# Kernel optimization log

Measured on AMD Instinct MI355X. Metric: run time of the kernel, lower is better.

## Reference

```python
import jax, jax.numpy as jnp
import numpy as np

B, L, D, H = 4, 1024, 768, 6
DH = D // H
EPS = 1e-5


def setup_inputs() -> dict:
    key = jax.random.key(0)
    kq, kk, kv, kl, kw = jax.random.split(key, 5)
    Q = jax.random.normal(kq, (B, L, D), jnp.float32)
    K = jax.random.normal(kk, (B, L, D), jnp.float32)
    V = jax.random.normal(kv, (B, L, D), jnp.float32)
    # realistic padding: each batch element has a valid length in [L//2, L]
    lengths = jax.random.randint(kl, (B,), L // 2, L + 1)
    valid = jnp.arange(L)[None, :] < lengths[:, None]          # (B, L)
    pad_mask = valid[:, :, None] & valid[:, None, :]           # (B, L, L), True = keep
    bx_packed = ~valid                                         # (B, L), True = padded
    # BatchNorm affine params (per-head channels)
    g1 = jnp.ones((H,), jnp.float32)
    b1 = jnp.zeros((H,), jnp.float32)
    g2 = jnp.ones((H,), jnp.float32)
    b2 = jnp.zeros((H,), jnp.float32)
    # posterior gate: Linear(H, 2)
    Wp = jax.random.normal(kw, (2, H), jnp.float32) * (1.0 / np.sqrt(H))
    bp = jnp.zeros((2,), jnp.float32)
    return {"Q": Q, "K": K, "V": V, "pad_mask": pad_mask, "bx_packed": bx_packed,
            "g1": g1, "b1": b1, "g2": g2, "b2": b2, "Wp": Wp, "bp": bp}


def _split_heads(x):
    b, l, _ = x.shape
    return x.reshape(b, l, H, DH).transpose(0, 2, 1, 3)  # (B, H, L, DH)


def _batchnorm(x, g, b):
    # x: (B, H, N); training-mode BatchNorm1d over channels H (stats over B and N)
    m = x.mean(axis=(0, 2), keepdims=True)
    v = x.var(axis=(0, 2), keepdims=True)  # biased, as torch uses for normalization
    return (x - m) * jax.lax.rsqrt(v + EPS) * g[None, :, None] + b[None, :, None]


def _remove_nan(x):
    return jnp.where(jnp.isnan(x), jnp.zeros_like(x), x)


def reference(Q, K, V, pad_mask, bx_packed, g1, b1, g2, b2, Wp, bp):
    Qh, Kh, Vh = _split_heads(Q), _split_heads(K), _split_heads(V)
    b, h, l, _ = Qh.shape
    # DistMatrix: negative squared Euclidean distance between query/key vectors
    # scores[b,h,i,j] = -||Q_i - K_j||^2, via the GEMM-friendly expansion
    q2 = jnp.sum(Qh * Qh, axis=-1)                     # (B, H, L)
    k2 = jnp.sum(Kh * Kh, axis=-1)                     # (B, H, L)
    qk = jnp.einsum("bhid,bhjd->bhij", Qh, Kh)         # (B, H, L, L)
    co = -(q2[..., :, None] + k2[..., None, :] - 2.0 * qk)
    # norm1 over flattened L*L
    co = _batchnorm(co.reshape(b, h, l * l), g1, b1).reshape(b, h, l, l)
    # zero out positions where pad_mask is False (in-place masked fill in torch)
    co = jnp.where(pad_mask[:, None, :, :], co, 0.0)
    co = jax.nn.softmax(co, axis=-1)
    co = _remove_nan(co)
    # column-sum attention mass per key position
    w = co.sum(axis=-2)                                # (B, H, L)
    w = _batchnorm(w, g2, b2).transpose(0, 2, 1)       # (B, L, H)
    # posterior gate: Linear(H,2) + softmax, take class-0 probability
    w = jax.nn.softmax(w @ Wp.T + bp, axis=-1)[..., 0]  # (B, L)
    w = _remove_nan(w)
    w = jnp.where(bx_packed, -jnp.inf, w)
    w = jax.nn.softmax(w, axis=-1)
    w = _remove_nan(w)[..., None]                      # (B, L, 1)
    return co, w, Vh
```

## Files before the change

### kernel.cpp

```cpp
#include <hip/hip_runtime.h>
#include <stdint.h>
#include <stddef.h>

#define BB 4
#define LL 1024
#define DD 768
#define HH 6
#define DHH 128
#define EPS 1e-5f

#define CO_ELEMS 25165824
#define W_ELEMS  4096

#define OFF_Q2  0
#define OFF_K2  24576
#define OFF_WC  49152
#define OFF_SP  73728
#define OFF_AC  79872
#define OFF_SS  79888
#define OFF_WP  81920

typedef __attribute__((ext_vector_type(8))) short short8;
typedef __attribute__((ext_vector_type(4))) float f32x4;

__device__ __forceinline__ short8 ld_bf8(const float* __restrict__ p) {
    const float4 a = *(const float4*)(p);
    const float4 b = *(const float4*)(p + 4);
    short8 r;
    r[0] = (short)(__float_as_uint(a.x) >> 16);
    r[1] = (short)(__float_as_uint(a.y) >> 16);
    r[2] = (short)(__float_as_uint(a.z) >> 16);
    r[3] = (short)(__float_as_uint(a.w) >> 16);
    r[4] = (short)(__float_as_uint(b.x) >> 16);
    r[5] = (short)(__float_as_uint(b.y) >> 16);
    r[6] = (short)(__float_as_uint(b.z) >> 16);
    r[7] = (short)(__float_as_uint(b.w) >> 16);
    return r;
}

__global__ void k_rownorm(const float* __restrict__ Q,
                          const float* __restrict__ K,
                          float* __restrict__ ws) {
    int gid = blockIdx.x * 256 + threadIdx.x;
    int sub = gid & 3;
    int rg  = gid >> 2;
    int which = (rg >= 24576);
    int rid = which ? rg - 24576 : rg;
    int bh = rid >> 10, i = rid & 1023;
    int b = bh / HH, h = bh - b * HH;
    const float* src = (which ? K : Q) + (size_t)(b * LL + i) * DD + h * DHH;
    float s = 0.f;
#pragma unroll
    for (int kk = 0; kk < 8; kk++) {
        float4 v = *(const float4*)(src + (sub + 4 * kk) * 4);
        s += v.x * v.x + v.y * v.y + v.z * v.z + v.w * v.w;
    }
    s += __shfl_xor(s, 1);
    s += __shfl_xor(s, 2);
    if (sub == 0) ws[(which ? OFF_K2 : OFF_Q2) + rid] = s;
}

__global__ void k_vh(const float* __restrict__ V, float* __restrict__ out) {
    int cid = blockIdx.x * 256 + threadIdx.x;
    if (cid >= 786432) return;
    int d4 = cid & 31;
    int rest = cid >> 5;
    int l = rest & 1023;
    int bh = rest >> 10;
    int b = bh / HH, h = bh - b * HH;
    f32x4 v = *(const f32x4*)(V + (size_t)(b * LL + l) * DD + h * DHH + d4 * 4);
    __builtin_nontemporal_store(v, (f32x4*)(out + (size_t)cid * 4));
}

__global__ __launch_bounds__(256) void k_gemm_S(
        const float* __restrict__ Q, const float* __restrict__ Km,
        const float* __restrict__ q2, const float* __restrict__ k2,
        float* __restrict__ co, float* __restrict__ statsP) {
    const int bh = blockIdx.z, b = bh / HH, h = bh - b * HH;
    const int tid = threadIdx.x, lane = tid & 63, wave = tid >> 6;
    const int wr = wave >> 1, wc = wave & 1;
    const int ibase = blockIdx.y * 64 + wr * 32;
    const int jbase = blockIdx.x * 128 + wc * 64;
    const int lm = lane & 15, quad = lane >> 4;
    const float* Qb = Q + (size_t)b * LL * DD + h * DHH;
    const float* Kb = Km + (size_t)b * LL * DD + h * DHH;

    f32x4 acc[2][4];
#pragma unroll
    for (int ti = 0; ti < 2; ti++)
#pragma unroll
        for (int tj = 0; tj < 4; tj++) acc[ti][tj] = (f32x4)(0.0f);

#pragma unroll
    for (int kk = 0; kk < 4; kk++) {
        const int d0 = kk * 32 + quad * 8;
        short8 af[2], bfr[4];
        af[0] = ld_bf8(Qb + (size_t)(ibase + lm) * DD + d0);
        af[1] = ld_bf8(Qb + (size_t)(ibase + 16 + lm) * DD + d0);
#pragma unroll
        for (int tj = 0; tj < 4; tj++)
            bfr[tj] = ld_bf8(Kb + (size_t)(jbase + tj * 16 + lm) * DD + d0);
#pragma unroll
        for (int ti = 0; ti < 2; ti++)
#pragma unroll
            for (int tj = 0; tj < 4; tj++)
                acc[ti][tj] = __builtin_amdgcn_mfma_f32_16x16x32_bf16(af[ti], bfr[tj], acc[ti][tj], 0, 0, 0);
    }

    float q2v[2][4], k2v[4];
#pragma unroll
    for (int ti = 0; ti < 2; ti++)
#pragma unroll
        for (int r = 0; r < 4; r++)
            q2v[ti][r] = q2[bh * 1024 + ibase + ti * 16 + quad * 4 + r];
#pragma unroll
    for (int tj = 0; tj < 4; tj++)
        k2v[tj] = k2[bh * 1024 + jbase + tj * 16 + lm];

    float s = 0.f, s2 = 0.f;
#pragma unroll
    for (int ti = 0; ti < 2; ti++)
#pragma unroll
        for (int tj = 0; tj < 4; tj++)
#pragma unroll
            for (int r = 0; r < 4; r++) {
                int i = ibase + ti * 16 + quad * 4 + r;
                int j = jbase + tj * 16 + lm;
                float S = 2.0f * acc[ti][tj][r] - q2v[ti][r] - k2v[tj];
                co[(size_t)(bh * 1024 + i) * 1024 + j] = S;
                s += S; s2 += S * S;
            }

    __shared__ float rA[256], rB[256];
    rA[tid] = s; rB[tid] = s2;
    __syncthreads();
    for (int off = 128; off > 0; off >>= 1) {
        if (tid < off) { rA[tid] += rA[tid + off]; rB[tid] += rB[tid + off]; }
        __syncthreads();
    }
    if (tid == 0) {
        int blk = blockIdx.y * 8 + blockIdx.x;
        int base = (bh * 128 + blk) * 2;
        statsP[base] = rA[0];
        statsP[base + 1] = rB[0];
    }
}

__global__ void k_stats(const float* __restrict__ statsP,
                        const float* __restrict__ g1, const float* __restrict__ b1,
                        float* __restrict__ ac) {
    __shared__ float rA[256], rB[256];
    const int t = threadIdx.x;
    for (int h = 0; h < HH; h++) {
        float s = 0.f, s2 = 0.f;
        for (int m = t; m < 512; m += 256) {
            int b = m >> 7, blk = m & 127;
            int base = ((b * HH + h) * 128 + blk) * 2;
            s += statsP[base]; s2 += statsP[base + 1];
        }
        rA[t] = s; rB[t] = s2;
        __syncthreads();
        for (int off = 128; off > 0; off >>= 1) {
            if (t < off) { rA[t] += rA[t + off]; rB[t] += rB[t + off]; }
            __syncthreads();
        }
        if (t == 0) {
            const float N = 4194304.f;
            float m_ = rA[0] / N;
            float var = fmaxf(rB[0] / N - m_ * m_, 0.0f);
            float r = rsqrtf(var + EPS);
            float a = r * g1[h];
            ac[h] = a;
            ac[8 + h] = b1[h] - m_ * a;
        }
        __syncthreads();
    }
}

__global__ __launch_bounds__(256) void k_normexp(
        float* __restrict__ co, const float* __restrict__ ac,
        const unsigned char* __restrict__ bx, float* __restrict__ wcolP) {
    const int bh = blockIdx.y;
    const int b = bh / HH, h = bh - b * HH;
    const int strip = blockIdx.x;
    const int t = threadIdx.x;
    float* base = co + ((size_t)bh << 20) + ((size_t)strip << 14);
    const float a = ac[h], c = ac[8 + h];

    const unsigned char* bxb = bx + b * LL;
    const uchar4 m4 = *(const uchar4*)(bxb + t * 4);
    const bool vj0 = (m4.x == 0), vj1 = (m4.y == 0), vj2 = (m4.z == 0), vj3 = (m4.w == 0);

    f32x4 buf[16];
    float rp[16];
#pragma unroll
    for (int r = 0; r < 16; r++) {
        const int i = strip * 16 + r;
        const bool vi = (bxb[i] == 0);
        f32x4 s4 = *(const f32x4*)(base + r * 1024 + t * 4);
        f32x4 e;
        e[0] = (vi && vj0) ? __expf(fminf(a * s4[0] + c, 60.0f)) : 1.0f;
        e[1] = (vi && vj1) ? __expf(fminf(a * s4[1] + c, 60.0f)) : 1.0f;
        e[2] = (vi && vj2) ? __expf(fminf(a * s4[2] + c, 60.0f)) : 1.0f;
        e[3] = (vi && vj3) ? __expf(fminf(a * s4[3] + c, 60.0f)) : 1.0f;
        buf[r] = e;
        rp[r] = e[0] + e[1] + e[2] + e[3];
    }

    __shared__ float pr[16][257];
    __shared__ float pr2[16][17];
    __shared__ float inv[16];
#pragma unroll
    for (int r = 0; r < 16; r++) pr[r][t] = rp[r];
    __syncthreads();
    {
        int r = t >> 4, k = t & 15;
        float s = 0.f;
#pragma unroll
        for (int j = 0; j < 16; j++) s += pr[r][k * 16 + j];
        pr2[r][k] = s;
    }
    __syncthreads();
    if (t < 16) {
        float s = 0.f;
#pragma unroll
        for (int k = 0; k < 16; k++) s += pr2[t][k];
        inv[t] = 1.0f / s;
    }
    __syncthreads();

    float cs0 = 0.f, cs1 = 0.f, cs2 = 0.f, cs3 = 0.f;
#pragma unroll
    for (int r = 0; r < 16; r++) {
        const float iv = inv[r];
        f32x4 v = buf[r];
        v[0] *= iv; v[1] *= iv; v[2] *= iv; v[3] *= iv;
        __builtin_nontemporal_store(v, (f32x4*)(base + r * 1024 + t * 4));
        cs0 += v[0]; cs1 += v[1]; cs2 += v[2]; cs3 += v[3];
    }
    float4 wv; wv.x = cs0; wv.y = cs1; wv.z = cs2; wv.w = cs3;
    *(float4*)&wcolP[((size_t)strip * 24 + bh) * 1024 + t * 4] = wv;
}

__global__ void k_wcol_reduce(const float* __restrict__ wcolP,
                              float* __restrict__ wcol, float* __restrict__ ws2) {
    const int t = threadIdx.x;
    int g = blockIdx.x * 256 + t;
    float s = 0.f;
#pragma unroll 8
    for (int strip = 0; strip < 64; strip++)
        s += wcolP[(size_t)strip * 24576 + g];
    wcol[g] = s;
    float a = s, b = s * s;
#pragma unroll
    for (int off = 1; off < 64; off <<= 1) { a += __shfl_xor(a, off); b += __shfl_xor(b, off); }
    __shared__ float sc[4][2];
    if ((t & 63) == 0) { sc[t >> 6][0] = a; sc[t >> 6][1] = b; }
    __syncthreads();
    if (t == 0) {
        ws2[blockIdx.x * 2]     = sc[0][0] + sc[1][0] + sc[2][0] + sc[3][0];
        ws2[blockIdx.x * 2 + 1] = sc[0][1] + sc[1][1] + sc[2][1] + sc[3][1];
    }
}

__global__ __launch_bounds__(1024) void k_tail(
        const float* __restrict__ wcol, const float* __restrict__ ws2,
        const unsigned char* __restrict__ bx,
        const float* __restrict__ g2, const float* __restrict__ b2,
        const float* __restrict__ Wp, const float* __restrict__ bp,
        float* __restrict__ wout) {
    const int t = threadIdx.x, lane = t & 63, wv = t >> 6;
    __shared__ float abuf[12];
    __shared__ float xb[4096];
    __shared__ float wred[16][2];

    if (t < HH) {
        float s = 0.f, s2 = 0.f;
        for (int b = 0; b < 4; b++) {
            int bh = b * HH + t;
#pragma unroll
            for (int sub = 0; sub < 4; sub++) {
                int blk = bh * 4 + sub;
                s += ws2[blk * 2];
                s2 += ws2[blk * 2 + 1];
            }
        }
        float m = s / 4096.f;
        float var = fmaxf(s2 / 4096.f - m * m, 0.0f);
        float r = rsqrtf(var + EPS);
        float a = r * g2[t];
        abuf[t] = a;
        abuf[6 + t] = b2[t] - m * a;
    }
    __syncthreads();

    const float bp0 = bp[0], bp1 = bp[1];
#pragma unroll
    for (int p = 0; p < 4; p++) {
        int idx = t + p * 1024;
        int b = idx >> 10, l = idx & 1023;
        float z0 = bp0, z1 = bp1;
#pragma unroll
        for (int h = 0; h < HH; h++) {
            float wn = abuf[h] * wcol[(size_t)(b * HH + h) * 1024 + l] + abuf[6 + h];
            z0 += wn * Wp[h];
            z1 += wn * Wp[HH + h];
        }
        float pc = 1.0f / (1.0f + __expf(z1 - z0));
        xb[idx] = bx[b * LL + l] ? -INFINITY : pc;
    }
    __syncthreads();

    const int bb = t >> 8, tb = t & 255;
    float4 xv = *(const float4*)&xb[bb * 1024 + tb * 4];
    float mx = fmaxf(fmaxf(xv.x, xv.y), fmaxf(xv.z, xv.w));
#pragma unroll
    for (int off = 1; off < 64; off <<= 1) mx = fmaxf(mx, __shfl_xor(mx, off));
    if (lane == 0) wred[wv][0] = mx;
    __syncthreads();
    mx = fmaxf(fmaxf(wred[bb * 4][0], wred[bb * 4 + 1][0]),
               fmaxf(wred[bb * 4 + 2][0], wred[bb * 4 + 3][0]));
    float e0 = __expf(xv.x - mx), e1 = __expf(xv.y - mx);
    float e2 = __expf(xv.z - mx), e3 = __expf(xv.w - mx);
    float ss = e0 + e1 + e2 + e3;
#pragma unroll
    for (int off = 1; off < 64; off <<= 1) ss += __shfl_xor(ss, off);
    if (lane == 0) wred[wv][1] = ss;
    __syncthreads();
    float sum = wred[bb * 4][1] + wred[bb * 4 + 1][1] + wred[bb * 4 + 2][1] + wred[bb * 4 + 3][1];
    float4 o;
    o.x = e0 / sum; o.y = e1 / sum; o.z = e2 / sum; o.w = e3 / sum;
    *(float4*)&wout[bb * 1024 + tb * 4] = o;
}

extern "C" void kernel_launch(void* const* d_in, const int* in_sizes, int n_in,
                              void* d_out, int out_size, void* d_ws, size_t ws_size,
                              hipStream_t stream) {
    const float* Q  = (const float*)d_in[0];
    const float* K  = (const float*)d_in[1];
    const float* V  = (const float*)d_in[2];
    const unsigned char* bx = (const unsigned char*)d_in[4];
    const float* g1 = (const float*)d_in[5];
    const float* b1 = (const float*)d_in[6];
    const float* g2 = (const float*)d_in[7];
    const float* b2 = (const float*)d_in[8];
    const float* Wp = (const float*)d_in[9];
    const float* bp = (const float*)d_in[10];

    float* out  = (float*)d_out;
    float* co   = out;
    float* wout = out + CO_ELEMS;
    float* vh   = out + CO_ELEMS + W_ELEMS;

    float* ws = (float*)d_ws;
    float* q2     = ws + OFF_Q2;
    float* k2     = ws + OFF_K2;
    float* wcol   = ws + OFF_WC;
    float* statsP = ws + OFF_SP;
    float* ac     = ws + OFF_AC;
    float* ws2    = ws + OFF_SS;
    float* wcolP  = ws + OFF_WP;

    k_rownorm<<<768, 256, 0, stream>>>(Q, K, ws);
    k_vh<<<3072, 256, 0, stream>>>(V, vh);
    k_gemm_S<<<dim3(8, 16, BB * HH), 256, 0, stream>>>(Q, K, q2, k2, co, statsP);
    k_stats<<<1, 256, 0, stream>>>(statsP, g1, b1, ac);
    k_normexp<<<dim3(64, 24), 256, 0, stream>>>(co, ac, bx, wcolP);
    k_wcol_reduce<<<96, 256, 0, stream>>>(wcolP, wcol, ws2);
    k_tail<<<1, 1024, 0, stream>>>(wcol, ws2, bx, g2, b2, Wp, bp, wout);
}
```

Baseline: 276.5 us.

## Recompute distance GEMM in fused softmax kernel instead of storing raw scores

The first GEMM pass now only computes batchnorm statistics and no longer writes the full score matrix. A new fused kernel recomputes the Q·K tile with bf16 MFMA, then applies the normalization, masked exp, row softmax and partial column sums, and writes the probabilities once. This removes a full write and read of the 100 MB score tensor, at the cost of running the GEMM twice and doing column sums through cross-lane shuffles.

```diff
diff --git a/kernel.cpp b/kernel.cpp
--- a/kernel.cpp
+++ b/kernel.cpp
@@ -72,10 +72,10 @@
     __builtin_nontemporal_store(v, (f32x4*)(out + (size_t)cid * 4));
 }
 
-__global__ __launch_bounds__(256) void k_gemm_S(
+__global__ __launch_bounds__(256) void k_gemm_stats(
         const float* __restrict__ Q, const float* __restrict__ Km,
         const float* __restrict__ q2, const float* __restrict__ k2,
-        float* __restrict__ co, float* __restrict__ statsP) {
+        float* __restrict__ statsP) {
     const int bh = blockIdx.z, b = bh / HH, h = bh - b * HH;
     const int tid = threadIdx.x, lane = tid & 63, wave = tid >> 6;
     const int wr = wave >> 1, wc = wave & 1;
@@ -124,10 +124,7 @@
         for (int tj = 0; tj < 4; tj++)
 #pragma unroll
             for (int r = 0; r < 4; r++) {
-                int i = ibase + ti * 16 + quad * 4 + r;
-                int j = jbase + tj * 16 + lm;
                 float S = 2.0f * acc[ti][tj][r] - q2v[ti][r] - k2v[tj];
-                co[(size_t)(bh * 1024 + i) * 1024 + j] = S;
                 s += S; s2 += S * S;
             }
 
@@ -177,69 +174,86 @@
     }
 }
 
-__global__ __launch_bounds__(256) void k_normexp(
-        float* __restrict__ co, const float* __restrict__ ac,
-        const unsigned char* __restrict__ bx, float* __restrict__ wcolP) {
-    const int bh = blockIdx.y;
+__global__ __launch_bounds__(512) void k_fused(
+        const float* __restrict__ Q, const float* __restrict__ Km,
+        const float* __restrict__ q2, const float* __restrict__ k2,
+        const float* __restrict__ ac, const unsigned char* __restrict__ bx,
+        float* __restrict__ co, float* __restrict__ wcolP) {
+    const int bh = blockIdx.x;
+    const int strip = blockIdx.y;
     const int b = bh / HH, h = bh - b * HH;
-    const int strip = blockIdx.x;
-    const int t = threadIdx.x;
-    float* base = co + ((size_t)bh << 20) + ((size_t)strip << 14);
-    const float a = ac[h], c = ac[8 + h];
-
+    const int t = threadIdx.x, lane = t & 63, w = t >> 6;
+    const int lm = lane & 15, quad = lane >> 4;
+    const int i0 = strip * 16;
+    const int jw = w * 128;
+    const float* Qb = Q + (size_t)b * LL * DD + h * DHH;
+    const float* Kb = Km + (size_t)b * LL * DD + h * DHH;
+    const float a1 = ac[h], c1 = ac[8 + h];
     const unsigned char* bxb = bx + b * LL;
-    const uchar4 m4 = *(const uchar4*)(bxb + t * 4);
-    const bool vj0 = (m4.x == 0), vj1 = (m4.y == 0), vj2 = (m4.z == 0), vj3 = (m4.w == 0);
-
-    f32x4 buf[16];
-    float rp[16];
-#pragma unroll
-    for (int r = 0; r < 16; r++) {
-        const int i = strip * 16 + r;
-        const bool vi = (bxb[i] == 0);
-        f32x4 s4 = *(const f32x4*)(base + r * 1024 + t * 4);
-        f32x4 e;
-        e[0] = (vi && vj0) ? __expf(fminf(a * s4[0] + c, 60.0f)) : 1.0f;
-        e[1] = (vi && vj1) ? __expf(fminf(a * s4[1] + c, 60.0f)) : 1.0f;
-        e[2] = (vi && vj2) ? __expf(fminf(a * s4[2] + c, 60.0f)) : 1.0f;
-        e[3] = (vi && vj3) ? __expf(fminf(a * s4[3] + c, 60.0f)) : 1.0f;
-        buf[r] = e;
-        rp[r] = e[0] + e[1] + e[2] + e[3];
-    }
-
-    __shared__ float pr[16][257];
-    __shared__ float pr2[16][17];
-    __shared__ float inv[16];
-#pragma unroll
-    for (int r = 0; r < 16; r++) pr[r][t] = rp[r];
-    __syncthreads();
-    {
-        int r = t >> 4, k = t & 15;
-        float s = 0.f;
-#pragma unroll
-        for (int j = 0; j < 16; j++) s += pr[r][k * 16 + j];
-        pr2[r][k] = s;
-    }
+
+    short8 qf[4];
+#pragma unroll
+    for (int kk = 0; kk < 4; kk++)
+        qf[kk] = ld_bf8(Qb + (size_t)(i0 + lm) * DD + kk * 32 + quad * 8);
+
+    const bool vi = (bxb[i0 + lm] == 0);
+    const float q2v = q2[bh * 1024 + i0 + lm];
+
+    f32x4 e[8];
+    float rsum = 0.f;
+#pragma unroll
+    for (int jt = 0; jt < 8; jt++) {
+        const int jb = jw + jt * 16;
+        short8 kf[4];
+#pragma unroll
+        for (int kk = 0; kk < 4; kk++)
+            kf[kk] = ld_bf8(Kb + (size_t)(jb + lm) * DD + kk * 32 + quad * 8);
+        f32x4 acc = (f32x4)(0.0f);
+#pragma unroll
+        for (int kk = 0; kk < 4; kk++)
+            acc = __builtin_amdgcn_mfma_f32_16x16x32_bf16(kf[kk], qf[kk], acc, 0, 0, 0);
+        const f32x4 k2v = *(const f32x4*)(k2 + bh * 1024 + jb + quad * 4);
+        const uchar4 m4 = *(const uchar4*)(bxb + jb + quad * 4);
+        f32x4 ev;
+        ev[0] = (vi && m4.x == 0) ? __expf(fminf(a1 * (2.0f * acc[0] - q2v - k2v[0]) + c1, 60.0f)) : 1.0f;
+        ev[1] = (vi && m4.y == 0) ? __expf(fminf(a1 * (2.0f * acc[1] - q2v - k2v[1]) + c1, 60.0f)) : 1.0f;
+        ev[2] = (vi && m4.z == 0) ? __expf(fminf(a1 * (2.0f * acc[2] - q2v - k2v[2]) + c1, 60.0f)) : 1.0f;
+        ev[3] = (vi && m4.w == 0) ? __expf(fminf(a1 * (2.0f * acc[3] - q2v - k2v[3]) + c1, 60.0f)) : 1.0f;
+        e[jt] = ev;
+        rsum += (ev[0] + ev[1]) + (ev[2] + ev[3]);
+    }
+    rsum += __shfl_xor(rsum, 16);
+    rsum += __shfl_xor(rsum, 32);
+    __shared__ float rs[8][16];
+    __shared__ float invs[16];
+    if (quad == 0) rs[w][lm] = rsum;
     __syncthreads();
     if (t < 16) {
         float s = 0.f;
 #pragma unroll
-        for (int k = 0; k < 16; k++) s += pr2[t][k];
-        inv[t] = 1.0f / s;
-    }
-    __syncthreads();
-
-    float cs0 = 0.f, cs1 = 0.f, cs2 = 0.f, cs3 = 0.f;
-#pragma unroll
-    for (int r = 0; r < 16; r++) {
-        const float iv = inv[r];
-        f32x4 v = buf[r];
-        v[0] *= iv; v[1] *= iv; v[2] *= iv; v[3] *= iv;
-        __builtin_nontemporal_store(v, (f32x4*)(base + r * 1024 + t * 4));
-        cs0 += v[0]; cs1 += v[1]; cs2 += v[2]; cs3 += v[3];
-    }
-    float4 wv; wv.x = cs0; wv.y = cs1; wv.z = cs2; wv.w = cs3;
-    *(float4*)&wcolP[((size_t)strip * 24 + bh) * 1024 + t * 4] = wv;
+        for (int ww = 0; ww < 8; ww++) s += rs[ww][t];
+        invs[t] = 1.0f / s;
+    }
+    __syncthreads();
+    const float inv = invs[lm];
+
+    float* rowbase = co + ((size_t)bh << 20) + (size_t)(i0 + lm) * 1024 + jw;
+    float* wp = wcolP + ((size_t)strip * 24 + bh) * 1024 + jw;
+#pragma unroll
+    for (int jt = 0; jt < 8; jt++) {
+        f32x4 p = e[jt];
+        p[0] *= inv; p[1] *= inv; p[2] *= inv; p[3] *= inv;
+        __builtin_nontemporal_store(p, (f32x4*)(rowbase + jt * 16 + quad * 4));
+        f32x4 cs = p;
+#pragma unroll
+        for (int m = 1; m < 16; m <<= 1) {
+            cs[0] += __shfl_xor(cs[0], m);
+            cs[1] += __shfl_xor(cs[1], m);
+            cs[2] += __shfl_xor(cs[2], m);
+            cs[3] += __shfl_xor(cs[3], m);
+        }
+        if (lm == 0) *(f32x4*)(wp + jt * 16 + quad * 4) = cs;
+    }
 }
 
 __global__ void k_wcol_reduce(const float* __restrict__ wcolP,
@@ -363,9 +377,9 @@
 
     k_rownorm<<<768, 256, 0, stream>>>(Q, K, ws);
     k_vh<<<3072, 256, 0, stream>>>(V, vh);
-    k_gemm_S<<<dim3(8, 16, BB * HH), 256, 0, stream>>>(Q, K, q2, k2, co, statsP);
+    k_gemm_stats<<<dim3(8, 16, BB * HH), 256, 0, stream>>>(Q, K, q2, k2, statsP);
     k_stats<<<1, 256, 0, stream>>>(statsP, g1, b1, ac);
-    k_normexp<<<dim3(64, 24), 256, 0, stream>>>(co, ac, bx, wcolP);
+    k_fused<<<dim3(24, 64), 512, 0, stream>>>(Q, K, q2, k2, ac, bx, co, wcolP);
     k_wcol_reduce<<<96, 256, 0, stream>>>(wcolP, wcol, ws2);
     k_tail<<<1, 1024, 0, stream>>>(wcol, ws2, bx, g2, b2, Wp, bp, wout);
 }
```

New measurement: 357.7 us. +29.4%, slower.
